# Performance work log

Measured on AMD Instinct MI355X. Metric: run time of the kernel, lower is better.

Reference implementation:

```python
import jax, jax.numpy as jnp
import numpy as np

NEG = -9e15
EPS = 1e-5

def setup_inputs() -> dict:
    key = jax.random.key(0)
    k1, k2, k3, k4 = jax.random.split(key, 4)
    B, S, D = 4, 2048, 1024
    q = jax.random.normal(k1, (B, S, D), dtype=jnp.float32)
    k = jax.random.normal(k2, (B, S, D), dtype=jnp.float32)
    v = jax.random.normal(k3, (B, S, D), dtype=jnp.float32)
    mask = jax.random.randint(k4, (B, S, S), 0, 2, dtype=jnp.int32)
    gamma = jnp.ones((D,), dtype=jnp.float32)
    beta = jnp.zeros((D,), dtype=jnp.float32)
    return {"q": q, "k": k, "v": v, "mask": mask, "gamma": gamma, "beta": beta}

def reference(q, k, v, mask, gamma, beta):
    d_k = q.shape[-1]
    # scaled dot-product attention: [B,S,S] logits materialized as in original
    logits = jnp.einsum('bsd,btd->bst', q, k) / jnp.sqrt(jnp.asarray(d_k, q.dtype))
    logits = jnp.where(mask == 0, jnp.asarray(NEG, logits.dtype), logits)
    attn = jax.nn.softmax(logits, axis=-1)
    x = jnp.einsum('bst,btd->bsd', attn, v)
    # dropout is identity at inference; LayerNorm over last dim
    mu = jnp.mean(x, axis=-1, keepdims=True)
    var = jnp.mean(jnp.square(x - mu), axis=-1, keepdims=True)
    xhat = (x - mu) * jax.lax.rsqrt(var + EPS)
    return xhat * gamma + beta
```

## Files before the change

### kernel.cpp

```cpp
#include <hip/hip_runtime.h>
#include <hip/hip_bf16.h>

typedef unsigned short u16;
typedef unsigned long long u64;
typedef __attribute__((ext_vector_type(8))) short bf16x8;
typedef __attribute__((ext_vector_type(4))) float f32x4;
typedef __attribute__((ext_vector_type(4))) float float4v;
typedef __attribute__((ext_vector_type(4))) short short4v;
typedef __attribute__((ext_vector_type(4))) int int4v;

#define BB 4
#define SS 2048
#define DD 1024

__device__ __forceinline__ u16 f2bf(float x){
    unsigned u = __float_as_uint(x);
    return (u16)((u + 0x7fffu + ((u >> 16) & 1u)) >> 16);
}

#define GLD16(g, l) __builtin_amdgcn_global_load_lds( \
    (const __attribute__((address_space(1))) unsigned int*)(g), \
    (__attribute__((address_space(3))) unsigned int*)(l), 16, 0, 0)

#define SCHED0() __builtin_amdgcn_sched_barrier(0)
#define PH_PRE()  SCHED0(); __builtin_amdgcn_s_barrier(); SCHED0(); __builtin_amdgcn_s_setprio(1)
#define PH_POST() __builtin_amdgcn_s_setprio(0); SCHED0(); __builtin_amdgcn_s_barrier(); SCHED0()

__global__ void conv_bf16_kernel(const float* __restrict__ in,
                                 u16* __restrict__ out, int n4, float scale){
    int i = blockIdx.x * 256 + threadIdx.x;
    if (i >= n4) return;
    float4v v = ((const float4v*)in)[i];
    short4v o;
    o[0] = (short)f2bf(v[0] * scale); o[1] = (short)f2bf(v[1] * scale);
    o[2] = (short)f2bf(v[2] * scale); o[3] = (short)f2bf(v[3] * scale);
    ((short4v*)out)[i] = o;
}

__global__ void transpose_v_kernel(const float* __restrict__ v,
                                   u16* __restrict__ vt){
    __shared__ float tile[64][65];
    const int b  = blockIdx.z;
    const int s0 = blockIdx.x << 6;
    const int d0 = blockIdx.y << 6;
    const int tx = threadIdx.x & 15;
    const int ty = threadIdx.x >> 4;
#pragma unroll
    for (int kk = 0; kk < 4; ++kk){
        const float* p = v + ((b * SS + s0 + ty + 16 * kk) * DD) + d0 + tx * 4;
        float4v val = *(const float4v*)p;
        tile[ty + 16 * kk][tx * 4 + 0] = val[0];
        tile[ty + 16 * kk][tx * 4 + 1] = val[1];
        tile[ty + 16 * kk][tx * 4 + 2] = val[2];
        tile[ty + 16 * kk][tx * 4 + 3] = val[3];
    }
    __syncthreads();
#pragma unroll
    for (int kk = 0; kk < 4; ++kk){
        int dy = ty + 16 * kk;
        short4v o;
        o[0] = (short)f2bf(tile[tx * 4 + 0][dy]);
        o[1] = (short)f2bf(tile[tx * 4 + 1][dy]);
        o[2] = (short)f2bf(tile[tx * 4 + 2][dy]);
        o[3] = (short)f2bf(tile[tx * 4 + 3][dy]);
        *(short4v*)&vt[((b * DD + d0 + dy) * SS) + s0 + tx * 4] = o;
    }
}

__global__ void zero_f32(float* __restrict__ p, int n){
    int i = blockIdx.x * 256 + threadIdx.x;
    if (i < n) p[i] = 0.f;
}

__global__ __launch_bounds__(256) void mask_pack_kernel(
    const int* __restrict__ m, unsigned int* __restrict__ bits){
    const int i = blockIdx.x * 256 + threadIdx.x;
    const int4v* p = (const int4v*)m + (size_t)i * 8;
    unsigned w = 0;
#pragma unroll
    for (int j = 0; j < 8; ++j){
        int4v v = p[j];
        w |= (unsigned)(v[0] != 0) << (j * 4 + 0);
        w |= (unsigned)(v[1] != 0) << (j * 4 + 1);
        w |= (unsigned)(v[2] != 0) << (j * 4 + 2);
        w |= (unsigned)(v[3] != 0) << (j * 4 + 3);
    }
    bits[i] = w;
}

__global__ __launch_bounds__(256, 2) void qk_kernel(
    const u16* __restrict__ Qb, const u16* __restrict__ Kb,
    const u64* __restrict__ mbits, u16* __restrict__ P,
    float* __restrict__ rowsum)
{
    __shared__ __align__(16) u16 Qs[2][128 * 64];
    __shared__ __align__(16) u16 Ks[2][128 * 64];

    const int swz = ((blockIdx.x & 7) << 7) + (blockIdx.x >> 3);
    const int b   = swz >> 8;
    const int bx  = (swz >> 4) & 15;
    const int by  = swz & 15;
    const int row0 = bx << 7, col0 = by << 7;

    const int tid = threadIdx.x;
    const int wid = tid >> 6, lane = tid & 63;
    const int l16 = lane & 15, g4 = lane >> 4;
    const int wq = wid >> 1, wk = wid & 1;

    const int sr   = tid >> 3;
    const int scol = ((tid & 7) ^ (sr & 7)) << 3;
    const u16* gA = Qb + (size_t)(b * SS + row0 + sr) * DD + scol;
    const u16* gB = Kb + (size_t)(b * SS + col0 + sr) * DD + scol;
    char* const lA0 = (char*)Qs[0] + tid * 16;
    char* const lB0 = (char*)Ks[0] + tid * 16;
    char* const lA1 = (char*)Qs[1] + tid * 16;
    char* const lB1 = (char*)Ks[1] + tid * 16;

    const int qRow = (wq * 64 + l16) << 7;
    const int kRow = (wk * 64 + l16) << 7;
    const int cx0  = (g4 << 4) ^ ((l16 & 7) << 4);

    f32x4 acc[4][4];
    const f32x4 z4 = {0.f, 0.f, 0.f, 0.f};
#pragma unroll
    for (int i = 0; i < 4; ++i)
#pragma unroll
        for (int j = 0; j < 4; ++j) acc[i][j] = z4;

#define STAGE_QK(kt, la, lb) { \
    const u16* ga_ = gA + (kt) * 64; \
    const u16* gb_ = gB + (kt) * 64; \
    GLD16(ga_,            (la)); \
    GLD16(ga_ + 32 * DD,  (la) + 4096); \
    GLD16(ga_ + 64 * DD,  (la) + 8192); \
    GLD16(ga_ + 96 * DD,  (la) + 12288); \
    GLD16(gb_,            (lb)); \
    GLD16(gb_ + 32 * DD,  (lb) + 4096); \
    GLD16(gb_ + 64 * DD,  (lb) + 8192); \
    GLD16(gb_ + 96 * DD,  (lb) + 12288); }

#define LDQ4(Qb_, kx) { \
    const char* p_ = (const char*)(Qb_) + qRow + ((kx) ? (cx0 ^ 64) : cx0); \
    fq0 = *(const bf16x8*)(p_); \
    fq1 = *(const bf16x8*)(p_ + 2048); \
    fq2 = *(const bf16x8*)(p_ + 4096); \
    fq3 = *(const bf16x8*)(p_ + 6144); }

#define LDK2(Kb_, mh, kx) { \
    const char* p_ = (const char*)(Kb_) + kRow + (mh) * 4096 + ((kx) ? (cx0 ^ 64) : cx0); \
    fk0 = *(const bf16x8*)(p_); \
    fk1 = *(const bf16x8*)(p_ + 2048); }

#define MKROW(mi, fk) \
    acc[mi][0] = __builtin_amdgcn_mfma_f32_16x16x32_bf16(fk, fq0, acc[mi][0],0,0,0); \
    acc[mi][1] = __builtin_amdgcn_mfma_f32_16x16x32_bf16(fk, fq1, acc[mi][1],0,0,0); \
    acc[mi][2] = __builtin_amdgcn_mfma_f32_16x16x32_bf16(fk, fq2, acc[mi][2],0,0,0); \
    acc[mi][3] = __builtin_amdgcn_mfma_f32_16x16x32_bf16(fk, fq3, acc[mi][3],0,0,0);

    STAGE_QK(0, lA0, lB0);
    STAGE_QK(1, lA1, lB1);
    asm volatile("s_waitcnt vmcnt(8)" ::: "memory");
    SCHED0(); __builtin_amdgcn_s_barrier(); SCHED0();

#pragma unroll 1
    for (int it = 0; it < 8; ++it){
        bf16x8 fq0, fq1, fq2, fq3, fk0, fk1;
        LDK2(Ks[0], 0, 0); LDQ4(Qs[0], 0);
        PH_PRE(); MKROW(0,fk0) MKROW(1,fk1) PH_POST();
        LDK2(Ks[0], 1, 0);
        PH_PRE(); MKROW(2,fk0) MKROW(3,fk1) PH_POST();
        LDK2(Ks[0], 0, 1); LDQ4(Qs[0], 1);
        PH_PRE(); MKROW(0,fk0) MKROW(1,fk1) PH_POST();
        LDK2(Ks[0], 1, 1);
        PH_PRE(); MKROW(2,fk0) MKROW(3,fk1) PH_POST();
        if (it < 7){
            STAGE_QK(2*it+2, lA0, lB0);
            asm volatile("s_waitcnt vmcnt(8)" ::: "memory");
        } else {
            asm volatile("s_waitcnt vmcnt(0)" ::: "memory");
        }
        SCHED0(); __builtin_amdgcn_s_barrier(); SCHED0();
        LDK2(Ks[1], 0, 0); LDQ4(Qs[1], 0);
        PH_PRE(); MKROW(0,fk0) MKROW(1,fk1) PH_POST();
        LDK2(Ks[1], 1, 0);
        PH_PRE(); MKROW(2,fk0) MKROW(3,fk1) PH_POST();
        LDK2(Ks[1], 0, 1); LDQ4(Qs[1], 1);
        PH_PRE(); MKROW(0,fk0) MKROW(1,fk1) PH_POST();
        LDK2(Ks[1], 1, 1);
        PH_PRE(); MKROW(2,fk0) MKROW(3,fk1) PH_POST();
        if (it < 7){
            STAGE_QK(2*it+3, lA1, lB1);
            asm volatile("s_waitcnt vmcnt(8)" ::: "memory");
            SCHED0(); __builtin_amdgcn_s_barrier(); SCHED0();
        }
    }
#undef STAGE_QK
#undef LDQ4
#undef LDK2
#undef MKROW

#pragma unroll
    for (int nq = 0; nq < 4; ++nq){
        const int grow = row0 + wq * 64 + nq * 16 + l16;
        const size_t rbase = (size_t)(b * SS + grow) * SS;
        const u64 w64 = mbits[(size_t)(b * SS + grow) * 32 + by * 2 + wk];
        float rs = 0.f;
#pragma unroll
        for (int mk = 0; mk < 4; ++mk){
            const int bit0 = mk * 16 + g4 * 4;
            const int gcolb = col0 + wk * 64 + bit0;
            float e0 = ((w64 >> (bit0 + 0)) & 1ull) ? __expf(acc[mk][nq][0]) : 0.f;
            float e1 = ((w64 >> (bit0 + 1)) & 1ull) ? __expf(acc[mk][nq][1]) : 0.f;
            float e2 = ((w64 >> (bit0 + 2)) & 1ull) ? __expf(acc[mk][nq][2]) : 0.f;
            float e3 = ((w64 >> (bit0 + 3)) & 1ull) ? __expf(acc[mk][nq][3]) : 0.f;
            short4v pp;
            pp[0] = (short)f2bf(e0); pp[1] = (short)f2bf(e1);
            pp[2] = (short)f2bf(e2); pp[3] = (short)f2bf(e3);
            *(short4v*)&P[rbase + gcolb] = pp;
            rs += (e0 + e1) + (e2 + e3);
        }
        rs += __shfl_xor(rs, 16);
        rs += __shfl_xor(rs, 32);
        if (g4 == 0) atomicAdd(&rowsum[b * SS + grow], rs);
    }
}

__global__ __launch_bounds__(512, 2) void pv_kernel(
    const u16* __restrict__ P, const u16* __restrict__ Vt,
    const float* __restrict__ rowsum, u16* __restrict__ Xn)
{
    __shared__ __align__(16) u16 As[2][128 * 64];
    __shared__ __align__(16) u16 Bs[2][256 * 64];

    const int swz = ((blockIdx.x & 7) << 5) + (blockIdx.x >> 3);
    const int b   = swz >> 6;
    const int bx  = (swz >> 2) & 15;
    const int by  = swz & 3;
    const int row0 = bx << 7, col0 = by << 8;

    const int tid = threadIdx.x;
    const int wid = tid >> 6, lane = tid & 63;
    const int l16 = lane & 15, g4 = lane >> 4;
    const int wr = wid >> 2, wc = wid & 3;

    const int sr   = tid >> 3;
    const int scol = ((tid & 7) ^ (sr & 7)) << 3;
    const u16* gA = P  + (size_t)(b * SS + row0 + sr) * SS + scol;
    const u16* gB = Vt + (size_t)(b * DD + col0 + sr) * SS + scol;
    char* const lA0 = (char*)As[0] + tid * 16;
    char* const lB0 = (char*)Bs[0] + tid * 16;
    char* const lA1 = (char*)As[1] + tid * 16;
    char* const lB1 = (char*)Bs[1] + tid * 16;

    const int aRow = (wr * 64 + l16) << 7;
    const int bRow = (wc * 64 + l16) << 7;
    const int cx0  = (g4 << 4) ^ ((l16 & 7) << 4);

    f32x4 acc[4][4];
    const f32x4 z4 = {0.f, 0.f, 0.f, 0.f};
#pragma unroll
    for (int i = 0; i < 4; ++i)
#pragma unroll
        for (int j = 0; j < 4; ++j) acc[i][j] = z4;

#define STAGE_PV(kt, la, lb) { \
    const u16* ga_ = gA + (kt) * 64; \
    const u16* gb_ = gB + (kt) * 64; \
    GLD16(ga_,            (la)); \
    GLD16(ga_ +  64 * SS, (la) + 8192); \
    GLD16(gb_,            (lb)); \
    GLD16(gb_ +  64 * SS, (lb) + 8192); \
    GLD16(gb_ + 128 * SS, (lb) + 16384); \
    GLD16(gb_ + 192 * SS, (lb) + 24576); }

#define LDA2(Ab_, mh, kx) { \
    const char* p_ = (const char*)(Ab_) + aRow + (mh) * 4096 + ((kx) ? (cx0 ^ 64) : cx0); \
    fa0 = *(const bf16x8*)(p_); \
    fa1 = *(const bf16x8*)(p_ + 2048); }

#define LDB4(Bb_, kx) { \
    const char* p_ = (const char*)(Bb_) + bRow + ((kx) ? (cx0 ^ 64) : cx0); \
    fb0 = *(const bf16x8*)(p_); \
    fb1 = *(const bf16x8*)(p_ + 2048); \
    fb2 = *(const bf16x8*)(p_ + 4096); \
    fb3 = *(const bf16x8*)(p_ + 6144); }

#define MROWP(mi, fa) \
    acc[mi][0] = __builtin_amdgcn_mfma_f32_16x16x32_bf16(fa, fb0, acc[mi][0],0,0,0); \
    acc[mi][1] = __builtin_amdgcn_mfma_f32_16x16x32_bf16(fa, fb1, acc[mi][1],0,0,0); \
    acc[mi][2] = __builtin_amdgcn_mfma_f32_16x16x32_bf16(fa, fb2, acc[mi][2],0,0,0); \
    acc[mi][3] = __builtin_amdgcn_mfma_f32_16x16x32_bf16(fa, fb3, acc[mi][3],0,0,0);

    STAGE_PV(0, lA0, lB0);
    STAGE_PV(1, lA1, lB1);
    asm volatile("s_waitcnt vmcnt(6)" ::: "memory");
    SCHED0(); __builtin_amdgcn_s_barrier(); SCHED0();

#pragma unroll 1
    for (int it = 0; it < 16; ++it){
        bf16x8 fa0, fa1, fb0, fb1, fb2, fb3;
        LDA2(As[0], 0, 0); LDB4(Bs[0], 0);
        PH_PRE(); MROWP(0,fa0) MROWP(1,fa1) PH_POST();
        LDA2(As[0], 1, 0);
        PH_PRE(); MROWP(2,fa0) MROWP(3,fa1) PH_POST();
        LDA2(As[0], 0, 1); LDB4(Bs[0], 1);
        PH_PRE(); MROWP(0,fa0) MROWP(1,fa1) PH_POST();
        LDA2(As[0], 1, 1);
        PH_PRE(); MROWP(2,fa0) MROWP(3,fa1) PH_POST();
        if (it < 15){
            STAGE_PV(2*it+2, lA0, lB0);
            asm volatile("s_waitcnt vmcnt(6)" ::: "memory");
        } else {
            asm volatile("s_waitcnt vmcnt(0)" ::: "memory");
        }
        SCHED0(); __builtin_amdgcn_s_barrier(); SCHED0();
        LDA2(As[1], 0, 0); LDB4(Bs[1], 0);
        PH_PRE(); MROWP(0,fa0) MROWP(1,fa1) PH_POST();
        LDA2(As[1], 1, 0);
        PH_PRE(); MROWP(2,fa0) MROWP(3,fa1) PH_POST();
        LDA2(As[1], 0, 1); LDB4(Bs[1], 1);
        PH_PRE(); MROWP(0,fa0) MROWP(1,fa1) PH_POST();
        LDA2(As[1], 1, 1);
        PH_PRE(); MROWP(2,fa0) MROWP(3,fa1) PH_POST();
        if (it < 15){
            STAGE_PV(2*it+3, lA1, lB1);
            asm volatile("s_waitcnt vmcnt(6)" ::: "memory");
            SCHED0(); __builtin_amdgcn_s_barrier(); SCHED0();
        }
    }
#undef STAGE_PV
#undef LDA2
#undef LDB4
#undef MROWP

#pragma unroll
    for (int m = 0; m < 4; ++m){
        float inv[4];
#pragma unroll
        for (int r = 0; r < 4; ++r)
            inv[r] = 1.f / rowsum[b * SS + row0 + wr * 64 + m * 16 + g4 * 4 + r];
#pragma unroll
        for (int n = 0; n < 4; ++n){
            const int gcol = col0 + wc * 64 + n * 16 + l16;
#pragma unroll
            for (int r = 0; r < 4; ++r){
                const int grow = row0 + wr * 64 + m * 16 + g4 * 4 + r;
                Xn[(size_t)(b * SS + grow) * DD + gcol] = f2bf(acc[m][n][r] * inv[r]);
            }
        }
    }
}

__global__ __launch_bounds__(256) void ln_kernel(
    const u16* __restrict__ Xn, const float* __restrict__ gamma,
    const float* __restrict__ beta, float* __restrict__ out)
{
    __shared__ float red[2][4];
    const int row = blockIdx.x;
    const int t = threadIdx.x;
    short4v xv = *(const short4v*)&Xn[(size_t)row * DD + t * 4];
    float x[4];
#pragma unroll
    for (int j = 0; j < 4; ++j)
        x[j] = __uint_as_float(((unsigned)(u16)xv[j]) << 16);
    float s  = x[0] + x[1] + x[2] + x[3];
    float sq = x[0]*x[0] + x[1]*x[1] + x[2]*x[2] + x[3]*x[3];
#pragma unroll
    for (int d = 1; d < 64; d <<= 1){ s += __shfl_xor(s, d); sq += __shfl_xor(sq, d); }
    const int wv = t >> 6;
    if ((t & 63) == 0){ red[0][wv] = s; red[1][wv] = sq; }
    __syncthreads();
    float S  = red[0][0] + red[0][1] + red[0][2] + red[0][3];
    float Sq = red[1][0] + red[1][1] + red[1][2] + red[1][3];
    float mu = S * (1.f / 1024.f);
    float var = Sq * (1.f / 1024.f) - mu * mu;
    float rstd = rsqrtf(var + 1e-5f);
    float4v g  = *(const float4v*)&gamma[t * 4];
    float4v be = *(const float4v*)&beta[t * 4];
    float4v o;
#pragma unroll
    for (int j = 0; j < 4; ++j) o[j] = (x[j] - mu) * rstd * g[j] + be[j];
    *(float4v*)&out[(size_t)row * DD + t * 4] = o;
}

extern "C" void kernel_launch(void* const* d_in, const int* in_sizes, int n_in,
                              void* d_out, int out_size, void* d_ws, size_t ws_size,
                              hipStream_t stream) {
    const float* q     = (const float*)d_in[0];
    const float* k     = (const float*)d_in[1];
    const float* v     = (const float*)d_in[2];
    const int*   mask  = (const int*)d_in[3];
    const float* gamma = (const float*)d_in[4];
    const float* beta  = (const float*)d_in[5];
    float* out = (float*)d_out;

    u16* Qb = (u16*)d_ws;
    u16* Kb = Qb + (size_t)BB * SS * DD;
    u16* Vt = Kb + (size_t)BB * SS * DD;
    u16* P  = Vt + (size_t)BB * SS * DD;
    u16* Xn = P  + (size_t)BB * SS * SS;
    float* rowsum = (float*)(Xn + (size_t)BB * SS * DD);
    unsigned int* mbits = (unsigned int*)Xn;

    const int n4 = BB * SS * DD / 4;
    conv_bf16_kernel<<<n4 / 256, 256, 0, stream>>>(q, Qb, n4, 0.03125f);
    conv_bf16_kernel<<<n4 / 256, 256, 0, stream>>>(k, Kb, n4, 1.0f);
    transpose_v_kernel<<<dim3(SS / 64, DD / 64, BB), 256, 0, stream>>>(v, Vt);
    zero_f32<<<BB * SS / 256, 256, 0, stream>>>(rowsum, BB * SS);
    mask_pack_kernel<<<(BB * SS * SS / 32) / 256, 256, 0, stream>>>(mask, mbits);

    qk_kernel<<<1024, 256, 0, stream>>>(Qb, Kb, (const u64*)mbits, P, rowsum);
    pv_kernel<<<256, 512, 0, stream>>>(P, Vt, rowsum, Xn);
    ln_kernel<<<BB * SS, 256, 0, stream>>>(Xn, gamma, beta, out);
}
```

Measured before the change: 152.8 us.

## Fuse preprocessing kernels into one launch and pack mask with wave ballots

Merges the Q/K bf16 conversion, V transpose, rowsum zeroing and mask bit-packing into a single prep kernel that dispatches on block index. This removes four kernel launches and their gaps. The mask packing now loads int4 vectors in a coalesced pattern and uses wave ballots, which produces an interleaved bit layout. The QK epilogue is rewritten to read four u64 words and pick bits with the matching shift arithmetic.

```diff
diff --git a/kernel.cpp b/kernel.cpp
--- a/kernel.cpp
+++ b/kernel.cpp
@@ -8,6 +8,7 @@
 typedef __attribute__((ext_vector_type(4))) float float4v;
 typedef __attribute__((ext_vector_type(4))) short short4v;
 typedef __attribute__((ext_vector_type(4))) int int4v;
+typedef __attribute__((ext_vector_type(4))) unsigned long long u64x4;
 
 #define BB 4
 #define SS 2048
@@ -26,71 +27,84 @@
 #define PH_PRE()  SCHED0(); __builtin_amdgcn_s_barrier(); SCHED0(); __builtin_amdgcn_s_setprio(1)
 #define PH_POST() __builtin_amdgcn_s_setprio(0); SCHED0(); __builtin_amdgcn_s_barrier(); SCHED0()
 
-__global__ void conv_bf16_kernel(const float* __restrict__ in,
-                                 u16* __restrict__ out, int n4, float scale){
-    int i = blockIdx.x * 256 + threadIdx.x;
-    if (i >= n4) return;
-    float4v v = ((const float4v*)in)[i];
-    short4v o;
-    o[0] = (short)f2bf(v[0] * scale); o[1] = (short)f2bf(v[1] * scale);
-    o[2] = (short)f2bf(v[2] * scale); o[3] = (short)f2bf(v[3] * scale);
-    ((short4v*)out)[i] = o;
-}
-
-__global__ void transpose_v_kernel(const float* __restrict__ v,
-                                   u16* __restrict__ vt){
-    __shared__ float tile[64][65];
-    const int b  = blockIdx.z;
-    const int s0 = blockIdx.x << 6;
-    const int d0 = blockIdx.y << 6;
-    const int tx = threadIdx.x & 15;
-    const int ty = threadIdx.x >> 4;
-#pragma unroll
-    for (int kk = 0; kk < 4; ++kk){
-        const float* p = v + ((b * SS + s0 + ty + 16 * kk) * DD) + d0 + tx * 4;
-        float4v val = *(const float4v*)p;
-        tile[ty + 16 * kk][tx * 4 + 0] = val[0];
-        tile[ty + 16 * kk][tx * 4 + 1] = val[1];
-        tile[ty + 16 * kk][tx * 4 + 2] = val[2];
-        tile[ty + 16 * kk][tx * 4 + 3] = val[3];
+__global__ __launch_bounds__(256) void prep_kernel(
+    const float* __restrict__ q, const float* __restrict__ k,
+    const float* __restrict__ v, const int* __restrict__ mask,
+    u16* __restrict__ Qb, u16* __restrict__ Kb, u16* __restrict__ Vt,
+    u64* __restrict__ mbits64, float* __restrict__ rowsum)
+{
+    const int bid = blockIdx.x;
+    const int tid = threadIdx.x;
+
+    if (bid < 4096){
+        const float* in = (bid < 2048) ? q : k;
+        u16* out = (bid < 2048) ? Qb : Kb;
+        const float scale = (bid < 2048) ? 0.03125f : 1.0f;
+        const int sb = bid & 2047;
+#pragma unroll
+        for (int kk = 0; kk < 4; ++kk){
+            int i = sb * 1024 + kk * 256 + tid;
+            float4v val = ((const float4v*)in)[i];
+            short4v o;
+            o[0] = (short)f2bf(val[0] * scale); o[1] = (short)f2bf(val[1] * scale);
+            o[2] = (short)f2bf(val[2] * scale); o[3] = (short)f2bf(val[3] * scale);
+            ((short4v*)out)[i] = o;
+        }
+    } else if (bid < 6144){
+        __shared__ float tile[64][65];
+        const int sb = bid - 4096;
+        const int b  = sb >> 9;
+        const int r  = sb & 511;
+        const int s0 = (r >> 4) << 6;
+        const int d0 = (r & 15) << 6;
+        const int tx = tid & 15;
+        const int ty = tid >> 4;
+#pragma unroll
+        for (int kk = 0; kk < 4; ++kk){
+            const float* p = v + ((size_t)(b * SS + s0 + ty + 16 * kk) * DD) + d0 + tx * 4;
+            float4v val = *(const float4v*)p;
+            tile[ty + 16 * kk][tx * 4 + 0] = val[0];
+            tile[ty + 16 * kk][tx * 4 + 1] = val[1];
+            tile[ty + 16 * kk][tx * 4 + 2] = val[2];
+            tile[ty + 16 * kk][tx * 4 + 3] = val[3];
+        }
+        __syncthreads();
+#pragma unroll
+        for (int kk = 0; kk < 4; ++kk){
+            int dy = ty + 16 * kk;
+            short4v o;
+            o[0] = (short)f2bf(tile[tx * 4 + 0][dy]);
+            o[1] = (short)f2bf(tile[tx * 4 + 1][dy]);
+            o[2] = (short)f2bf(tile[tx * 4 + 2][dy]);
+            o[3] = (short)f2bf(tile[tx * 4 + 3][dy]);
+            *(short4v*)&Vt[((size_t)(b * DD + d0 + dy) * SS) + s0 + tx * 4] = o;
+        }
+    } else if (bid < 8192){
+        const int sb = bid - 6144;
+        const int tt = sb * 256 + tid;
+        const int lane = tid & 63;
+#pragma unroll
+        for (int j = 0; j < 8; ++j){
+            const int idx = j * 524288 + tt;
+            int4v mm = ((const int4v*)mask)[idx];
+            u64 b0 = __ballot(mm[0] != 0);
+            u64 b1 = __ballot(mm[1] != 0);
+            u64 b2 = __ballot(mm[2] != 0);
+            u64 b3 = __ballot(mm[3] != 0);
+            const int gw = idx >> 6;
+            if (lane < 4){
+                u64 w = (lane == 0) ? b0 : (lane == 1) ? b1 : (lane == 2) ? b2 : b3;
+                mbits64[(size_t)gw * 4 + lane] = w;
+            }
+        }
+    } else {
+        rowsum[(bid - 8192) * 256 + tid] = 0.f;
     }
-    __syncthreads();
-#pragma unroll
-    for (int kk = 0; kk < 4; ++kk){
-        int dy = ty + 16 * kk;
-        short4v o;
-        o[0] = (short)f2bf(tile[tx * 4 + 0][dy]);
-        o[1] = (short)f2bf(tile[tx * 4 + 1][dy]);
-        o[2] = (short)f2bf(tile[tx * 4 + 2][dy]);
-        o[3] = (short)f2bf(tile[tx * 4 + 3][dy]);
-        *(short4v*)&vt[((b * DD + d0 + dy) * SS) + s0 + tx * 4] = o;
-    }
-}
-
-__global__ void zero_f32(float* __restrict__ p, int n){
-    int i = blockIdx.x * 256 + threadIdx.x;
-    if (i < n) p[i] = 0.f;
-}
-
-__global__ __launch_bounds__(256) void mask_pack_kernel(
-    const int* __restrict__ m, unsigned int* __restrict__ bits){
-    const int i = blockIdx.x * 256 + threadIdx.x;
-    const int4v* p = (const int4v*)m + (size_t)i * 8;
-    unsigned w = 0;
-#pragma unroll
-    for (int j = 0; j < 8; ++j){
-        int4v v = p[j];
-        w |= (unsigned)(v[0] != 0) << (j * 4 + 0);
-        w |= (unsigned)(v[1] != 0) << (j * 4 + 1);
-        w |= (unsigned)(v[2] != 0) << (j * 4 + 2);
-        w |= (unsigned)(v[3] != 0) << (j * 4 + 3);
-    }
-    bits[i] = w;
 }
 
 __global__ __launch_bounds__(256, 2) void qk_kernel(
     const u16* __restrict__ Qb, const u16* __restrict__ Kb,
-    const u64* __restrict__ mbits, u16* __restrict__ P,
+    const u64* __restrict__ mbits64, u16* __restrict__ P,
     float* __restrict__ rowsum)
 {
     __shared__ __align__(16) u16 Qs[2][128 * 64];
@@ -199,20 +213,22 @@
 #undef LDK2
 #undef MKROW
 
+    const int m = (by << 1) | wk;
+    const int shbase = ((m & 3) << 4) + g4;
 #pragma unroll
     for (int nq = 0; nq < 4; ++nq){
         const int grow = row0 + wq * 64 + nq * 16 + l16;
         const size_t rbase = (size_t)(b * SS + grow) * SS;
-        const u64 w64 = mbits[(size_t)(b * SS + grow) * 32 + by * 2 + wk];
+        u64x4 w = *(const u64x4*)&mbits64[((size_t)(b * SS + grow) * 8 + (m >> 2)) * 4];
         float rs = 0.f;
 #pragma unroll
         for (int mk = 0; mk < 4; ++mk){
-            const int bit0 = mk * 16 + g4 * 4;
-            const int gcolb = col0 + wk * 64 + bit0;
-            float e0 = ((w64 >> (bit0 + 0)) & 1ull) ? __expf(acc[mk][nq][0]) : 0.f;
-            float e1 = ((w64 >> (bit0 + 1)) & 1ull) ? __expf(acc[mk][nq][1]) : 0.f;
-            float e2 = ((w64 >> (bit0 + 2)) & 1ull) ? __expf(acc[mk][nq][2]) : 0.f;
-            float e3 = ((w64 >> (bit0 + 3)) & 1ull) ? __expf(acc[mk][nq][3]) : 0.f;
+            const int sh = shbase + (mk << 2);
+            const int gcolb = col0 + wk * 64 + mk * 16 + g4 * 4;
+            float e0 = ((w[0] >> sh) & 1ull) ? __expf(acc[mk][nq][0]) : 0.f;
+            float e1 = ((w[1] >> sh) & 1ull) ? __expf(acc[mk][nq][1]) : 0.f;
+            float e2 = ((w[2] >> sh) & 1ull) ? __expf(acc[mk][nq][2]) : 0.f;
+            float e3 = ((w[3] >> sh) & 1ull) ? __expf(acc[mk][nq][3]) : 0.f;
             short4v pp;
             pp[0] = (short)f2bf(e0); pp[1] = (short)f2bf(e1);
             pp[2] = (short)f2bf(e2); pp[3] = (short)f2bf(e3);
@@ -400,16 +416,10 @@
     u16* P  = Vt + (size_t)BB * SS * DD;
     u16* Xn = P  + (size_t)BB * SS * SS;
     float* rowsum = (float*)(Xn + (size_t)BB * SS * DD);
-    unsigned int* mbits = (unsigned int*)Xn;
-
-    const int n4 = BB * SS * DD / 4;
-    conv_bf16_kernel<<<n4 / 256, 256, 0, stream>>>(q, Qb, n4, 0.03125f);
-    conv_bf16_kernel<<<n4 / 256, 256, 0, stream>>>(k, Kb, n4, 1.0f);
-    transpose_v_kernel<<<dim3(SS / 64, DD / 64, BB), 256, 0, stream>>>(v, Vt);
-    zero_f32<<<BB * SS / 256, 256, 0, stream>>>(rowsum, BB * SS);
-    mask_pack_kernel<<<(BB * SS * SS / 32) / 256, 256, 0, stream>>>(mask, mbits);
-
-    qk_kernel<<<1024, 256, 0, stream>>>(Qb, Kb, (const u64*)mbits, P, rowsum);
+    u64* mbits64 = (u64*)Xn;
+
+    prep_kernel<<<8224, 256, 0, stream>>>(q, k, v, mask, Qb, Kb, Vt, mbits64, rowsum);
+    qk_kernel<<<1024, 256, 0, stream>>>(Qb, Kb, mbits64, P, rowsum);
     pv_kernel<<<256, 512, 0, stream>>>(P, Vt, rowsum, Xn);
     ln_kernel<<<BB * SS, 256, 0, stream>>>(Xn, gamma, beta, out);
 }
```

Result: faster. 141.1 us (-7.6%).
